# Kernel optimization log

Measured on AMD Instinct MI355X. Metric: run time of the kernel, lower is better.

Reference implementation:

```python
import jax, jax.numpy as jnp
import numpy as np

V = 500000   # num_vertexes
T = 4        # edge_type_num
D = 32       # edge_embedding_size
E = 128      # embedding_size
A = 32       # attention_dim
B = 8192     # batch
S = 10       # neighbor_samples


def setup_inputs() -> dict:
    key = jax.random.key(0)
    ks = jax.random.split(key, 8)
    glorot = lambda k, shape: jax.random.normal(k, shape, dtype=jnp.float32) * np.sqrt(2.0 / (shape[-2] + shape[-1])).astype(np.float32)
    return {
        "targets": jax.random.randint(ks[0], (B,), 0, V, dtype=jnp.int32),
        "types": jax.random.randint(ks[1], (B,), 0, T, dtype=jnp.int32),
        "neighbors": jax.random.randint(ks[2], (B, T, S), 0, V, dtype=jnp.int32),
        "base_node_embeddings": jax.random.uniform(ks[3], (V, E), minval=-1.0, maxval=1.0, dtype=jnp.float32),
        "node_type_embeddings": jax.random.uniform(ks[4], (V, T, D), minval=-1.0, maxval=1.0, dtype=jnp.float32),
        "trans_weights": glorot(ks[5], (T, D, E)),
        "trans_weights_s1": glorot(ks[6], (T, D, A)),
        "trans_weights_s2": glorot(ks[7], (T, A, 1)),
    }


def reference(targets, types, neighbors,
              base_node_embeddings, node_type_embeddings,
              trans_weights, trans_weights_s1, trans_weights_s2):
    # TF code gathers [B,T,S,T,D] then slices the (i,i) diagonal per edge type.
    # Equivalent, cheaper: per edge type i, gather node_type_embeddings[:, i, :]
    # at neighbors[:, i, :].  vmap over the edge-type axis.
    nte_t = jnp.transpose(node_type_embeddings, (1, 0, 2))          # [T,V,D]
    gathered = jax.vmap(lambda emb_t, nb_t: emb_t[nb_t],
                        in_axes=(0, 1))(nte_t, neighbors)           # [T,B,S,D]
    node_agg = jnp.transpose(gathered.mean(axis=2), (1, 0, 2))      # [B,T,D]

    tw  = trans_weights[types]       # [B,D,E]
    tw1 = trans_weights_s1[types]    # [B,D,A]
    tw2 = trans_weights_s2[types]    # [B,A,1]

    u = jnp.tanh(jnp.einsum('btd,bda->bta', node_agg, tw1))         # [B,T,A]
    scores = jnp.einsum('bta,bao->bto', u, tw2)[..., 0]             # [B,T]
    att = jax.nn.softmax(scores, axis=-1)                           # [B,T]
    node_att = jnp.einsum('bt,btd->bd', att, node_agg)              # [B,D]
    proj = jnp.einsum('bd,bde->be', node_att, tw)                   # [B,E]

    all_node_embed = base_node_embeddings[targets] + proj           # [B,E]
    # tf.nn.l2_normalize: x * rsqrt(max(sum(x^2), 1e-12))
    sq = jnp.sum(all_node_embed * all_node_embed, axis=1, keepdims=True)
    embeddings = all_node_embed * jax.lax.rsqrt(jnp.maximum(sq, 1e-12))
    return embeddings
```

## Files before the change

kernel.cpp:

```cpp
#include <hip/hip_runtime.h>
#include <hip/hip_bf16.h>


constexpr int TT = 4;
constexpr int DD = 32;
constexpr int EE = 128;
constexpr int AA = 32;
constexpr int SS = 10;

__global__ __launch_bounds__(128) void gatne_fused(
    const int*   __restrict__ targets,
    const int*   __restrict__ types,
    const int*   __restrict__ neighbors,
    const float* __restrict__ base_emb,
    const float* __restrict__ nte,
    const float* __restrict__ tw,
    const float* __restrict__ tw1,
    const float* __restrict__ tw2,
    float*       __restrict__ out)
{
    const int b    = blockIdx.x;
    const int tid  = threadIdx.x;
    const int t    = tid >> 5;
    const int lane = tid & 31;

    __shared__ float s_agg[TT][DD];
    __shared__ float s_scores[TT];
    __shared__ float s_natt[DD];
    __shared__ int   s_nb[TT * SS];
    __shared__ int   s_meta[2];
    __shared__ float s_part[2];
    __shared__ float s_inv;

    if (tid == 0) s_meta[0] = types[b];
    if (tid == 1) s_meta[1] = targets[b];
    if (tid < TT * SS) s_nb[tid] = neighbors[b * (TT * SS) + tid];
    __syncthreads();

    const int ty = s_meta[0];
    const int tg = s_meta[1];

    float acc = 0.f;
    #pragma unroll
    for (int s = 0; s < SS; ++s) {
        const int v = s_nb[t * SS + s];
        acc += nte[(long long)v * (TT * DD) + t * DD + lane];
    }
    s_agg[t][lane] = acc * 0.1f;
    __syncthreads();

    float ua = 0.f;
    #pragma unroll
    for (int d = 0; d < DD; ++d)
        ua += s_agg[t][d] * tw1[ty * (DD * AA) + d * AA + lane];
    ua = tanhf(ua);

    float p = ua * tw2[ty * AA + lane];
    #pragma unroll
    for (int m = 16; m >= 1; m >>= 1)
        p += __shfl_xor(p, m, 64);
    if (lane == 0) s_scores[t] = p;
    __syncthreads();

    const float sc0 = s_scores[0], sc1 = s_scores[1];
    const float sc2 = s_scores[2], sc3 = s_scores[3];
    const float mx  = fmaxf(fmaxf(sc0, sc1), fmaxf(sc2, sc3));
    const float e0 = expf(sc0 - mx), e1 = expf(sc1 - mx);
    const float e2 = expf(sc2 - mx), e3 = expf(sc3 - mx);
    const float inv_sum = 1.f / (e0 + e1 + e2 + e3);

    if (tid < DD) {
        const float na = (e0 * s_agg[0][tid] + e1 * s_agg[1][tid] +
                          e2 * s_agg[2][tid] + e3 * s_agg[3][tid]) * inv_sum;
        s_natt[tid] = na;
    }
    __syncthreads();

    float val = 0.f;
    #pragma unroll
    for (int d = 0; d < DD; ++d)
        val += s_natt[d] * tw[ty * (DD * EE) + d * EE + tid];
    val += base_emb[(long long)tg * EE + tid];

    float sq = val * val;
    #pragma unroll
    for (int m = 32; m >= 1; m >>= 1)
        sq += __shfl_xor(sq, m, 64);
    if ((tid & 63) == 0) s_part[tid >> 6] = sq;
    __syncthreads();
    if (tid == 0) s_inv = rsqrtf(fmaxf(s_part[0] + s_part[1], 1e-12f));
    __syncthreads();

    out[b * EE + tid] = val * s_inv;
}

extern "C" void kernel_launch(void* const* d_in, const int* in_sizes, int n_in,
                              void* d_out, int out_size, void* d_ws, size_t ws_size,
                              hipStream_t stream) {
    const int*   targets   = (const int*)d_in[0];
    const int*   types     = (const int*)d_in[1];
    const int*   neighbors = (const int*)d_in[2];
    const float* base_emb  = (const float*)d_in[3];
    const float* nte       = (const float*)d_in[4];
    const float* tw        = (const float*)d_in[5];
    const float* tw1       = (const float*)d_in[6];
    const float* tw2       = (const float*)d_in[7];
    float*       out       = (float*)d_out;

    const int B = in_sizes[0];
    (void)n_in; (void)out_size; (void)d_ws; (void)ws_size;

    gatne_fused<<<B, 128, 0, stream>>>(targets, types, neighbors,
                                       base_emb, nte, tw, tw1, tw2, out);
}
```

Baseline: 410.5 us.

## Vectorize neighbor gather with float4 loads and shuffle reduction, prefetch base embedding

```diff
diff --git a/kernel.cpp b/kernel.cpp
--- a/kernel.cpp
+++ b/kernel.cpp
@@ -19,60 +19,71 @@
     const float* __restrict__ tw2,
     float*       __restrict__ out)
 {
-    const int b    = blockIdx.x;
-    const int tid  = threadIdx.x;
-    const int t    = tid >> 5;
-    const int lane = tid & 31;
+    const int b   = blockIdx.x;
+    const int tid = threadIdx.x;
+    const int g   = tid >> 3;
+    const int li  = tid & 7;
+    const int t   = g >> 2;
+    const int j   = g & 3;
 
     __shared__ float s_agg[TT][DD];
     __shared__ float s_scores[TT];
     __shared__ float s_natt[DD];
-    __shared__ int   s_nb[TT * SS];
-    __shared__ int   s_meta[2];
     __shared__ float s_part[2];
-    __shared__ float s_inv;
 
-    if (tid == 0) s_meta[0] = types[b];
-    if (tid == 1) s_meta[1] = targets[b];
-    if (tid < TT * SS) s_nb[tid] = neighbors[b * (TT * SS) + tid];
+    const int ty = types[b];
+    const int tg = targets[b];
+    const float bval = base_emb[(long long)tg * EE + tid];
+
+    const int base_nb = b * (TT * SS) + t * SS;
+    const int v0 = neighbors[base_nb + j];
+    const int v1 = neighbors[base_nb + j + 4];
+    const int v2 = (j < 2) ? neighbors[base_nb + j + 8] : 0;
+
+    const float4* __restrict__ nte4 = (const float4*)nte;
+    const int fo = t * 8 + li;
+    float4 a0 = nte4[(long long)v0 * 32 + fo];
+    float4 a1 = nte4[(long long)v1 * 32 + fo];
+    float ax = a0.x + a1.x, ay = a0.y + a1.y, az = a0.z + a1.z, aw = a0.w + a1.w;
+    if (j < 2) {
+        float4 a2 = nte4[(long long)v2 * 32 + fo];
+        ax += a2.x; ay += a2.y; az += a2.z; aw += a2.w;
+    }
+    ax += __shfl_xor(ax, 8, 64);  ay += __shfl_xor(ay, 8, 64);
+    az += __shfl_xor(az, 8, 64);  aw += __shfl_xor(aw, 8, 64);
+    ax += __shfl_xor(ax, 16, 64); ay += __shfl_xor(ay, 16, 64);
+    az += __shfl_xor(az, 16, 64); aw += __shfl_xor(aw, 16, 64);
+    if (j == 0) {
+        float4 m = make_float4(ax * 0.1f, ay * 0.1f, az * 0.1f, aw * 0.1f);
+        ((float4*)&s_agg[t][0])[li] = m;
+    }
     __syncthreads();
 
-    const int ty = s_meta[0];
-    const int tg = s_meta[1];
-
-    float acc = 0.f;
-    #pragma unroll
-    for (int s = 0; s < SS; ++s) {
-        const int v = s_nb[t * SS + s];
-        acc += nte[(long long)v * (TT * DD) + t * DD + lane];
-    }
-    s_agg[t][lane] = acc * 0.1f;
-    __syncthreads();
-
+    const int t2   = tid >> 5;
+    const int lane = tid & 31;
     float ua = 0.f;
     #pragma unroll
     for (int d = 0; d < DD; ++d)
-        ua += s_agg[t][d] * tw1[ty * (DD * AA) + d * AA + lane];
+        ua += s_agg[t2][d] * tw1[ty * (DD * AA) + d * AA + lane];
     ua = tanhf(ua);
 
     float p = ua * tw2[ty * AA + lane];
     #pragma unroll
     for (int m = 16; m >= 1; m >>= 1)
         p += __shfl_xor(p, m, 64);
-    if (lane == 0) s_scores[t] = p;
+    if (lane == 0) s_scores[t2] = p;
     __syncthreads();
 
     const float sc0 = s_scores[0], sc1 = s_scores[1];
     const float sc2 = s_scores[2], sc3 = s_scores[3];
     const float mx  = fmaxf(fmaxf(sc0, sc1), fmaxf(sc2, sc3));
-    const float e0 = expf(sc0 - mx), e1 = expf(sc1 - mx);
-    const float e2 = expf(sc2 - mx), e3 = expf(sc3 - mx);
+    const float e0 = __expf(sc0 - mx), e1 = __expf(sc1 - mx);
+    const float e2 = __expf(sc2 - mx), e3 = __expf(sc3 - mx);
     const float inv_sum = 1.f / (e0 + e1 + e2 + e3);
 
     if (tid < DD) {
-        const float na = (e0 * s_agg[0][tid] + e1 * s_agg[1][tid] +
-                          e2 * s_agg[2][tid] + e3 * s_agg[3][tid]) * inv_sum;
-        s_natt[tid] = na;
+        s_natt[tid] = (e0 * s_agg[0][tid] + e1 * s_agg[1][tid] +
+                       e2 * s_agg[2][tid] + e3 * s_agg[3][tid]) * inv_sum;
     }
     __syncthreads();
 
@@ -80,7 +91,7 @@
     #pragma unroll
     for (int d = 0; d < DD; ++d)
         val += s_natt[d] * tw[ty * (DD * EE) + d * EE + tid];
-    val += base_emb[(long long)tg * EE + tid];
+    val += bval;
 
     float sq = val * val;
     #pragma unroll
@@ -88,10 +99,9 @@
         sq += __shfl_xor(sq, m, 64);
     if ((tid & 63) == 0) s_part[tid >> 6] = sq;
     __syncthreads();
-    if (tid == 0) s_inv = rsqrtf(fmaxf(s_part[0] + s_part[1], 1e-12f));
-    __syncthreads();
+    const float inv = rsqrtf(fmaxf(s_part[0] + s_part[1], 1e-12f));
 
-    out[b * EE + tid] = val * s_inv;
+    out[b * EE + tid] = val * inv;
 }
 
 extern "C" void kernel_launch(void* const* d_in, const int* in_sizes, int n_in,
```

New measurement: 411.3 us. Within noise of the previous version (+0.2%).
